# Kernel optimization log

Measured on AMD Instinct MI355X. Metric: run time of the kernel, lower is better.

## Reference

```python
import jax, jax.numpy as jnp
import numpy as np

COMMITMENT_COST = 0.25
NUM_EMBEDDINGS = 512
EMBEDDING_DIM = 64


def setup_inputs() -> dict:
    key = jax.random.key(0)
    k1, k2 = jax.random.split(key)
    inputs = jax.random.normal(k1, (32, EMBEDDING_DIM, 64, 64), dtype=jnp.float32)  # B,C,H,W
    embedding = jax.random.normal(k2, (NUM_EMBEDDINGS, EMBEDDING_DIM), dtype=jnp.float32)  # K,D
    return {"inputs": inputs, "embedding": embedding}


def reference(inputs, embedding):
    # Eval-mode forward of VectorQuantizerEMA (training-branch EMA updates are
    # in-place buffer updates, skipped when self.training is False).
    x = jnp.transpose(inputs, (0, 2, 3, 1))            # B,H,W,C
    B, H, W, D = x.shape
    K = embedding.shape[0]
    flat = x.reshape(-1, D)                            # N,D
    d = (jnp.sum(flat * flat, axis=1, keepdims=True)
         + jnp.sum(embedding * embedding, axis=1)
         - 2.0 * flat @ embedding.T)
    indices = jnp.argmin(d, axis=1)                    # N (int)
    # gather == one-hot @ embedding, but without materializing N x K one-hot
    quantized = embedding[indices].reshape(B, H, W, D)
    # commitment loss (quantized is detached in the torch code)
    e_latent_loss = jnp.mean((jax.lax.stop_gradient(quantized) - x) ** 2)
    loss = COMMITMENT_COST * e_latent_loss
    # straight-through estimator
    quantized_st = x + jax.lax.stop_gradient(quantized - x)
    # perplexity from encoding histogram (avg of one-hots = counts / N)
    counts = jnp.zeros((K,), dtype=flat.dtype).at[indices].add(1.0)
    avg_probs = counts / flat.shape[0]
    perplexity = jnp.exp(-jnp.sum(avg_probs * jnp.log(avg_probs + 1e-10)))
    out = jnp.transpose(quantized_st, (0, 3, 1, 2))    # B,C,H,W
    return loss, out, perplexity, indices
```

## Files before the change

### kernel.cpp

```cpp
#include <hip/hip_runtime.h>
#include <math.h>

#define NPIX   131072
#define KEMB   512
#define DDIM   64
#define HW     4096
#define BSTRIDE 262144

#define OUT_OFF  1
#define PERP_OFF 8388609
#define IDX_OFF  8388610

typedef __attribute__((ext_vector_type(8))) short bf16x8;
typedef __attribute__((ext_vector_type(4))) float f32x4;

__device__ __forceinline__ unsigned short bf16_rtne(float f) {
    unsigned int u = __float_as_uint(f);
    u += 0x7FFFu + ((u >> 16) & 1u);
    return (unsigned short)(u >> 16);
}
__device__ __forceinline__ float bf16_to_f(unsigned short h) {
    return __uint_as_float(((unsigned int)h) << 16);
}

__global__ void vq_init(const float* __restrict__ emb, int* __restrict__ counts,
                        float* __restrict__ hnorms, float* __restrict__ loss_acc,
                        unsigned short* __restrict__ ebh, unsigned short* __restrict__ ebm,
                        unsigned short* __restrict__ ebl) {
    int k = blockIdx.x * 64 + threadIdx.x;
    counts[k] = 0;
    const float4* row4 = (const float4*)(emb + k * DDIM);
    float s = 0.f;
#pragma unroll
    for (int i = 0; i < 16; ++i) {
        float4 v = row4[i];
        s += v.x * v.x + v.y * v.y + v.z * v.z + v.w * v.w;
    }
    hnorms[k] = 0.5f * s;
    const float* row = emb + k * DDIM;
#pragma unroll
    for (int c = 0; c < DDIM; ++c) {
        float x = row[c];
        unsigned short h = bf16_rtne(x);
        float r1 = x - bf16_to_f(h);
        unsigned short m = bf16_rtne(r1);
        float r2 = r1 - bf16_to_f(m);
        unsigned short l = bf16_rtne(r2);
        ebh[k * DDIM + c] = h; ebm[k * DDIM + c] = m; ebl[k * DDIM + c] = l;
    }
    if (k == 0) *loss_acc = 0.f;
}

__global__ __launch_bounds__(256, 2) void vq_main(
    const float* __restrict__ in, const float* __restrict__ emb,
    const unsigned short* __restrict__ ebh, const unsigned short* __restrict__ ebm,
    const unsigned short* __restrict__ ebl,
    const float* __restrict__ hnorms, int* __restrict__ counts,
    float* __restrict__ loss_acc, float* __restrict__ dout)
{
    __shared__ int hist[KEMB];
    const int t = threadIdx.x;
    hist[t] = 0; hist[t + 256] = 0;
    __syncthreads();

    const int lane = t & 63;
    const int wid  = t >> 6;
    const int quad = lane >> 4;
    const int col  = lane & 15;
    const int b    = blockIdx.x >> 4;
    const int p0   = ((blockIdx.x & 15) << 8) | (wid << 6);
    const float* xb = in + b * BSTRIDE;

    bf16x8 xf[3][4][2];
#pragma unroll
    for (int tt = 0; tt < 4; ++tt) {
#pragma unroll
        for (int s = 0; s < 2; ++s) {
            const int pp = p0 + tt * 16 + col;
            const int c0 = s * 32 + quad * 8;
            bf16x8 vh, vm, vl;
#pragma unroll
            for (int j = 0; j < 8; ++j) {
                float x = xb[(c0 + j) * HW + pp];
                unsigned short h = bf16_rtne(x);
                float r1 = x - bf16_to_f(h);
                unsigned short m = bf16_rtne(r1);
                float r2 = r1 - bf16_to_f(m);
                unsigned short l = bf16_rtne(r2);
                vh[j] = (short)h; vm[j] = (short)m; vl[j] = (short)l;
            }
            xf[0][tt][s] = vh; xf[1][tt][s] = vm; xf[2][tt][s] = vl;
        }
    }

    const int arow = col * DDIM + quad * 8;

    float v1[4], v2[4]; int k1[4], k2[4];
#pragma unroll
    for (int tt = 0; tt < 4; ++tt) {
        v1[tt] = 3.402823466e38f; v2[tt] = 3.402823466e38f; k1[tt] = 0; k2[tt] = 0;
    }

#pragma unroll 2
    for (int ct = 0; ct < 32; ++ct) {
        const int off = ct * 16 * DDIM + arow;
        const bf16x8 Ah0 = *(const bf16x8*)(ebh + off);
        const bf16x8 Ah1 = *(const bf16x8*)(ebh + off + 32);
        const bf16x8 Am0 = *(const bf16x8*)(ebm + off);
        const bf16x8 Am1 = *(const bf16x8*)(ebm + off + 32);
        const bf16x8 Al0 = *(const bf16x8*)(ebl + off);
        const bf16x8 Al1 = *(const bf16x8*)(ebl + off + 32);

        f32x4 acc[4];
#pragma unroll
        for (int tt = 0; tt < 4; ++tt) acc[tt] = (f32x4){0.f, 0.f, 0.f, 0.f};

#pragma unroll
        for (int tt = 0; tt < 4; ++tt) {
            acc[tt] = __builtin_amdgcn_mfma_f32_16x16x32_bf16(Ah0, xf[0][tt][0], acc[tt], 0, 0, 0);
            acc[tt] = __builtin_amdgcn_mfma_f32_16x16x32_bf16(Ah0, xf[1][tt][0], acc[tt], 0, 0, 0);
            acc[tt] = __builtin_amdgcn_mfma_f32_16x16x32_bf16(Am0, xf[0][tt][0], acc[tt], 0, 0, 0);
            acc[tt] = __builtin_amdgcn_mfma_f32_16x16x32_bf16(Ah0, xf[2][tt][0], acc[tt], 0, 0, 0);
            acc[tt] = __builtin_amdgcn_mfma_f32_16x16x32_bf16(Al0, xf[0][tt][0], acc[tt], 0, 0, 0);
            acc[tt] = __builtin_amdgcn_mfma_f32_16x16x32_bf16(Am0, xf[1][tt][0], acc[tt], 0, 0, 0);
            acc[tt] = __builtin_amdgcn_mfma_f32_16x16x32_bf16(Ah1, xf[0][tt][1], acc[tt], 0, 0, 0);
            acc[tt] = __builtin_amdgcn_mfma_f32_16x16x32_bf16(Ah1, xf[1][tt][1], acc[tt], 0, 0, 0);
            acc[tt] = __builtin_amdgcn_mfma_f32_16x16x32_bf16(Am1, xf[0][tt][1], acc[tt], 0, 0, 0);
            acc[tt] = __builtin_amdgcn_mfma_f32_16x16x32_bf16(Ah1, xf[2][tt][1], acc[tt], 0, 0, 0);
            acc[tt] = __builtin_amdgcn_mfma_f32_16x16x32_bf16(Al1, xf[0][tt][1], acc[tt], 0, 0, 0);
            acc[tt] = __builtin_amdgcn_mfma_f32_16x16x32_bf16(Am1, xf[1][tt][1], acc[tt], 0, 0, 0);
        }

        const f32x4 hn = *(const f32x4*)(hnorms + ct * 16 + quad * 4);
#pragma unroll
        for (int tt = 0; tt < 4; ++tt) {
#pragma unroll
            for (int r = 0; r < 4; ++r) {
                const float sc = hn[r] - acc[tt][r];
                const int   kk = ct * 16 + quad * 4 + r;
                if (sc < v1[tt]) { v2[tt] = v1[tt]; k2[tt] = k1[tt]; v1[tt] = sc; k1[tt] = kk; }
                else if (sc < v2[tt]) { v2[tt] = sc; k2[tt] = kk; }
            }
        }
    }

#pragma unroll
    for (int tt = 0; tt < 4; ++tt) {
#pragma unroll
        for (int off = 16; off <= 32; off <<= 1) {
            float w1 = __shfl_xor(v1[tt], off, 64); int j1 = __shfl_xor(k1[tt], off, 64);
            float w2 = __shfl_xor(v2[tt], off, 64); int j2 = __shfl_xor(k2[tt], off, 64);
            bool aF = (v1[tt] < w1) || (v1[tt] == w1 && k1[tt] < j1);
            float t1 = aF ? v1[tt] : w1;  int u1 = aF ? k1[tt] : j1;
            float tl = aF ? w1 : v1[tt];  int ul = aF ? j1 : k1[tt];
            bool bS = (v2[tt] < w2) || (v2[tt] == w2 && k2[tt] < j2);
            float tc = bS ? v2[tt] : w2;  int uc = bS ? k2[tt] : j2;
            bool lS = (tl < tc) || (tl == tc && ul < uc);
            v1[tt] = t1; k1[tt] = u1;
            v2[tt] = lS ? tl : tc; k2[tt] = lS ? ul : uc;
        }
    }
    const int kA = k1[quad], kB = k2[quad];
    const int pp = p0 + lane;

    float x[DDIM];
#pragma unroll
    for (int c = 0; c < DDIM; ++c) x[c] = xb[c * HW + pp];

    const float4* eA = (const float4*)(emb + kA * DDIM);
    const float4* eB = (const float4*)(emb + kB * DDIM);
    float a0 = hnorms[kA], a1 = 0.f, a2 = 0.f, a3 = 0.f;
    float b0 = hnorms[kB], b1 = 0.f, b2 = 0.f, b3 = 0.f;
#pragma unroll
    for (int i = 0; i < 16; ++i) {
        float4 ea = eA[i], eb = eB[i];
        const int c = i * 4;
        a0 = fmaf(-x[c + 0], ea.x, a0);
        a1 = fmaf(-x[c + 1], ea.y, a1);
        a2 = fmaf(-x[c + 2], ea.z, a2);
        a3 = fmaf(-x[c + 3], ea.w, a3);
        b0 = fmaf(-x[c + 0], eb.x, b0);
        b1 = fmaf(-x[c + 1], eb.y, b1);
        b2 = fmaf(-x[c + 2], eb.z, b2);
        b3 = fmaf(-x[c + 3], eb.w, b3);
    }
    const float dA = (a0 + a1) + (a2 + a3);
    const float dB = (b0 + b1) + (b2 + b3);
    const int myk = (dB < dA || (dB == dA && kB < kA)) ? kB : kA;

    dout[IDX_OFF + b * HW + pp] = (float)myk;
    atomicAdd(&hist[myk], 1);

    const float4* qrow = (const float4*)(emb + myk * DDIM);
    float* ob = dout + OUT_OFF + b * BSTRIDE;
    float lsum = 0.f;
#pragma unroll
    for (int i = 0; i < 16; ++i) {
        float4 qv = qrow[i];
        const int c = i * 4;
        float d0 = qv.x - x[c + 0];
        float d1 = qv.y - x[c + 1];
        float d2 = qv.z - x[c + 2];
        float d3 = qv.w - x[c + 3];
        lsum += d0 * d0 + d1 * d1 + d2 * d2 + d3 * d3;
        ob[(c + 0) * HW + pp] = x[c + 0] + d0;
        ob[(c + 1) * HW + pp] = x[c + 1] + d1;
        ob[(c + 2) * HW + pp] = x[c + 2] + d2;
        ob[(c + 3) * HW + pp] = x[c + 3] + d3;
    }
    for (int off = 32; off > 0; off >>= 1) lsum += __shfl_down(lsum, off, 64);
    if (lane == 0) atomicAdd(loss_acc, lsum);

    __syncthreads();
    for (int k = t; k < KEMB; k += 256) {
        int v = hist[k];
        if (v) atomicAdd(&counts[k], v);
    }
}

__global__ void vq_fin(const int* __restrict__ counts,
                       const float* __restrict__ loss_acc,
                       float* __restrict__ dout) {
    __shared__ float red[KEMB];
    int k = threadIdx.x;
    float c = (float)counts[k];
    float pa = c / (float)NPIX;
    red[k] = pa * logf(pa + 1e-10f);
    __syncthreads();
    for (int s = 256; s > 0; s >>= 1) {
        if (k < s) red[k] += red[k + s];
        __syncthreads();
    }
    if (k == 0) {
        dout[PERP_OFF] = expf(-red[0]);
        dout[0] = 0.25f * (*loss_acc) / 8388608.0f;
    }
}

extern "C" void kernel_launch(void* const* d_in, const int* in_sizes, int n_in,
                              void* d_out, int out_size, void* d_ws, size_t ws_size,
                              hipStream_t stream) {
    const float* in  = (const float*)d_in[0];
    const float* emb = (const float*)d_in[1];
    float* dout = (float*)d_out;
    int*   counts   = (int*)d_ws;
    float* hnorms   = (float*)((char*)d_ws + 2048);
    float* loss_acc = (float*)((char*)d_ws + 4096);
    unsigned short* ebh = (unsigned short*)((char*)d_ws + 8192);
    unsigned short* ebm = ebh + KEMB * DDIM;
    unsigned short* ebl = ebm + KEMB * DDIM;

    vq_init<<<8, 64, 0, stream>>>(emb, counts, hnorms, loss_acc, ebh, ebm, ebl);
    vq_main<<<512, 256, 0, stream>>>(in, emb, ebh, ebm, ebl, hnorms, counts, loss_acc, dout);
    vq_fin<<<1, 512, 0, stream>>>(counts, loss_acc, dout);
}
```

Baseline: 184.2 us.

## Halve pixels per wave, double grid, prefetch codebook tiles, split refine across lanes

Each wave now handles 32 pixels instead of 64, so the main kernel launches 1024 blocks, and launch bounds are raised to allow 3 blocks per SM. The codebook tile loop is software-pipelined so the next tile's split-bf16 fragments load while the current tile's MFMAs run. The exact fp32 refine of the top two candidates is split across lane halves with a shuffle. vq_init is also parallelized to one thread per element. This trades more blocks and twice the codebook reads per pixel for better occupancy and latency hiding, and half the lanes sit idle during the output write.

```diff
diff --git a/kernel.cpp b/kernel.cpp
--- a/kernel.cpp
+++ b/kernel.cpp
@@ -23,35 +23,38 @@
     return __uint_as_float(((unsigned int)h) << 16);
 }
 
+#define MFMA_STEP(AH, AM, AL, XH, XM, XL, ACC) \
+    ACC = __builtin_amdgcn_mfma_f32_16x16x32_bf16(AH, XH, ACC, 0, 0, 0); \
+    ACC = __builtin_amdgcn_mfma_f32_16x16x32_bf16(AH, XM, ACC, 0, 0, 0); \
+    ACC = __builtin_amdgcn_mfma_f32_16x16x32_bf16(AM, XH, ACC, 0, 0, 0); \
+    ACC = __builtin_amdgcn_mfma_f32_16x16x32_bf16(AH, XL, ACC, 0, 0, 0); \
+    ACC = __builtin_amdgcn_mfma_f32_16x16x32_bf16(AL, XH, ACC, 0, 0, 0); \
+    ACC = __builtin_amdgcn_mfma_f32_16x16x32_bf16(AM, XM, ACC, 0, 0, 0);
+
 __global__ void vq_init(const float* __restrict__ emb, int* __restrict__ counts,
                         float* __restrict__ hnorms, float* __restrict__ loss_acc,
                         unsigned short* __restrict__ ebh, unsigned short* __restrict__ ebm,
                         unsigned short* __restrict__ ebl) {
-    int k = blockIdx.x * 64 + threadIdx.x;
-    counts[k] = 0;
-    const float4* row4 = (const float4*)(emb + k * DDIM);
-    float s = 0.f;
-#pragma unroll
-    for (int i = 0; i < 16; ++i) {
-        float4 v = row4[i];
-        s += v.x * v.x + v.y * v.y + v.z * v.z + v.w * v.w;
-    }
-    hnorms[k] = 0.5f * s;
-    const float* row = emb + k * DDIM;
-#pragma unroll
-    for (int c = 0; c < DDIM; ++c) {
-        float x = row[c];
-        unsigned short h = bf16_rtne(x);
-        float r1 = x - bf16_to_f(h);
-        unsigned short m = bf16_rtne(r1);
-        float r2 = r1 - bf16_to_f(m);
-        unsigned short l = bf16_rtne(r2);
-        ebh[k * DDIM + c] = h; ebm[k * DDIM + c] = m; ebl[k * DDIM + c] = l;
-    }
-    if (k == 0) *loss_acc = 0.f;
-}
-
-__global__ __launch_bounds__(256, 2) void vq_main(
+    const int k = blockIdx.x;
+    const int c = threadIdx.x;
+    float x = emb[k * DDIM + c];
+    unsigned short h = bf16_rtne(x);
+    float r1 = x - bf16_to_f(h);
+    unsigned short m = bf16_rtne(r1);
+    float r2 = r1 - bf16_to_f(m);
+    unsigned short l = bf16_rtne(r2);
+    ebh[k * DDIM + c] = h; ebm[k * DDIM + c] = m; ebl[k * DDIM + c] = l;
+    float s = x * x;
+#pragma unroll
+    for (int off = 1; off <= 32; off <<= 1) s += __shfl_xor(s, off, 64);
+    if (c == 0) {
+        hnorms[k] = 0.5f * s;
+        counts[k] = 0;
+        if (k == 0) *loss_acc = 0.f;
+    }
+}
+
+__global__ __launch_bounds__(256, 3) void vq_main(
     const float* __restrict__ in, const float* __restrict__ emb,
     const unsigned short* __restrict__ ebh, const unsigned short* __restrict__ ebm,
     const unsigned short* __restrict__ ebl,
@@ -67,13 +70,13 @@
     const int wid  = t >> 6;
     const int quad = lane >> 4;
     const int col  = lane & 15;
-    const int b    = blockIdx.x >> 4;
-    const int p0   = ((blockIdx.x & 15) << 8) | (wid << 6);
+    const int b    = blockIdx.x >> 5;
+    const int p0   = ((blockIdx.x & 31) << 7) | (wid << 5);
     const float* xb = in + b * BSTRIDE;
 
-    bf16x8 xf[3][4][2];
-#pragma unroll
-    for (int tt = 0; tt < 4; ++tt) {
+    bf16x8 xf[3][2][2];
+#pragma unroll
+    for (int tt = 0; tt < 2; ++tt) {
 #pragma unroll
         for (int s = 0; s < 2; ++s) {
             const int pp = p0 + tt * 16 + col;
@@ -95,57 +98,76 @@
 
     const int arow = col * DDIM + quad * 8;
 
-    float v1[4], v2[4]; int k1[4], k2[4];
-#pragma unroll
-    for (int tt = 0; tt < 4; ++tt) {
+    float v1[2], v2[2]; int k1[2], k2[2];
+#pragma unroll
+    for (int tt = 0; tt < 2; ++tt) {
         v1[tt] = 3.402823466e38f; v2[tt] = 3.402823466e38f; k1[tt] = 0; k2[tt] = 0;
     }
 
-#pragma unroll 2
-    for (int ct = 0; ct < 32; ++ct) {
-        const int off = ct * 16 * DDIM + arow;
-        const bf16x8 Ah0 = *(const bf16x8*)(ebh + off);
-        const bf16x8 Ah1 = *(const bf16x8*)(ebh + off + 32);
-        const bf16x8 Am0 = *(const bf16x8*)(ebm + off);
-        const bf16x8 Am1 = *(const bf16x8*)(ebm + off + 32);
-        const bf16x8 Al0 = *(const bf16x8*)(ebl + off);
-        const bf16x8 Al1 = *(const bf16x8*)(ebl + off + 32);
-
-        f32x4 acc[4];
-#pragma unroll
-        for (int tt = 0; tt < 4; ++tt) acc[tt] = (f32x4){0.f, 0.f, 0.f, 0.f};
-
-#pragma unroll
-        for (int tt = 0; tt < 4; ++tt) {
-            acc[tt] = __builtin_amdgcn_mfma_f32_16x16x32_bf16(Ah0, xf[0][tt][0], acc[tt], 0, 0, 0);
-            acc[tt] = __builtin_amdgcn_mfma_f32_16x16x32_bf16(Ah0, xf[1][tt][0], acc[tt], 0, 0, 0);
-            acc[tt] = __builtin_amdgcn_mfma_f32_16x16x32_bf16(Am0, xf[0][tt][0], acc[tt], 0, 0, 0);
-            acc[tt] = __builtin_amdgcn_mfma_f32_16x16x32_bf16(Ah0, xf[2][tt][0], acc[tt], 0, 0, 0);
-            acc[tt] = __builtin_amdgcn_mfma_f32_16x16x32_bf16(Al0, xf[0][tt][0], acc[tt], 0, 0, 0);
-            acc[tt] = __builtin_amdgcn_mfma_f32_16x16x32_bf16(Am0, xf[1][tt][0], acc[tt], 0, 0, 0);
-            acc[tt] = __builtin_amdgcn_mfma_f32_16x16x32_bf16(Ah1, xf[0][tt][1], acc[tt], 0, 0, 0);
-            acc[tt] = __builtin_amdgcn_mfma_f32_16x16x32_bf16(Ah1, xf[1][tt][1], acc[tt], 0, 0, 0);
-            acc[tt] = __builtin_amdgcn_mfma_f32_16x16x32_bf16(Am1, xf[0][tt][1], acc[tt], 0, 0, 0);
-            acc[tt] = __builtin_amdgcn_mfma_f32_16x16x32_bf16(Ah1, xf[2][tt][1], acc[tt], 0, 0, 0);
-            acc[tt] = __builtin_amdgcn_mfma_f32_16x16x32_bf16(Al1, xf[0][tt][1], acc[tt], 0, 0, 0);
-            acc[tt] = __builtin_amdgcn_mfma_f32_16x16x32_bf16(Am1, xf[1][tt][1], acc[tt], 0, 0, 0);
-        }
-
-        const f32x4 hn = *(const f32x4*)(hnorms + ct * 16 + quad * 4);
-#pragma unroll
-        for (int tt = 0; tt < 4; ++tt) {
-#pragma unroll
-            for (int r = 0; r < 4; ++r) {
-                const float sc = hn[r] - acc[tt][r];
-                const int   kk = ct * 16 + quad * 4 + r;
-                if (sc < v1[tt]) { v2[tt] = v1[tt]; k2[tt] = k1[tt]; v1[tt] = sc; k1[tt] = kk; }
-                else if (sc < v2[tt]) { v2[tt] = sc; k2[tt] = kk; }
-            }
-        }
-    }
-
-#pragma unroll
-    for (int tt = 0; tt < 4; ++tt) {
+    bf16x8 Ah0 = *(const bf16x8*)(ebh + arow);
+    bf16x8 Ah1 = *(const bf16x8*)(ebh + arow + 32);
+    bf16x8 Am0 = *(const bf16x8*)(ebm + arow);
+    bf16x8 Am1 = *(const bf16x8*)(ebm + arow + 32);
+    bf16x8 Al0 = *(const bf16x8*)(ebl + arow);
+    bf16x8 Al1 = *(const bf16x8*)(ebl + arow + 32);
+    f32x4 hnA = *(const f32x4*)(hnorms + quad * 4);
+
+    for (int ct = 0; ct < 32; ct += 2) {
+        const int offB = (ct + 1) * (16 * DDIM) + arow;
+        const bf16x8 Bh0 = *(const bf16x8*)(ebh + offB);
+        const bf16x8 Bh1 = *(const bf16x8*)(ebh + offB + 32);
+        const bf16x8 Bm0 = *(const bf16x8*)(ebm + offB);
+        const bf16x8 Bm1 = *(const bf16x8*)(ebm + offB + 32);
+        const bf16x8 Bl0 = *(const bf16x8*)(ebl + offB);
+        const bf16x8 Bl1 = *(const bf16x8*)(ebl + offB + 32);
+        const f32x4 hnB = *(const f32x4*)(hnorms + (ct + 1) * 16 + quad * 4);
+
+        f32x4 acc0 = (f32x4){0.f, 0.f, 0.f, 0.f};
+        f32x4 acc1 = (f32x4){0.f, 0.f, 0.f, 0.f};
+        MFMA_STEP(Ah0, Am0, Al0, xf[0][0][0], xf[1][0][0], xf[2][0][0], acc0)
+        MFMA_STEP(Ah1, Am1, Al1, xf[0][0][1], xf[1][0][1], xf[2][0][1], acc0)
+        MFMA_STEP(Ah0, Am0, Al0, xf[0][1][0], xf[1][1][0], xf[2][1][0], acc1)
+        MFMA_STEP(Ah1, Am1, Al1, xf[0][1][1], xf[1][1][1], xf[2][1][1], acc1)
+#pragma unroll
+        for (int r = 0; r < 4; ++r) {
+            const int kk = ct * 16 + quad * 4 + r;
+            float sc = hnA[r] - acc0[r];
+            if (sc < v1[0]) { v2[0] = v1[0]; k2[0] = k1[0]; v1[0] = sc; k1[0] = kk; }
+            else if (sc < v2[0]) { v2[0] = sc; k2[0] = kk; }
+            sc = hnA[r] - acc1[r];
+            if (sc < v1[1]) { v2[1] = v1[1]; k2[1] = k1[1]; v1[1] = sc; k1[1] = kk; }
+            else if (sc < v2[1]) { v2[1] = sc; k2[1] = kk; }
+        }
+
+        const int offA = (((ct + 2) & 31)) * (16 * DDIM) + arow;
+        Ah0 = *(const bf16x8*)(ebh + offA);
+        Ah1 = *(const bf16x8*)(ebh + offA + 32);
+        Am0 = *(const bf16x8*)(ebm + offA);
+        Am1 = *(const bf16x8*)(ebm + offA + 32);
+        Al0 = *(const bf16x8*)(ebl + offA);
+        Al1 = *(const bf16x8*)(ebl + offA + 32);
+        hnA = *(const f32x4*)(hnorms + ((ct + 2) & 31) * 16 + quad * 4);
+
+        acc0 = (f32x4){0.f, 0.f, 0.f, 0.f};
+        acc1 = (f32x4){0.f, 0.f, 0.f, 0.f};
+        MFMA_STEP(Bh0, Bm0, Bl0, xf[0][0][0], xf[1][0][0], xf[2][0][0], acc0)
+        MFMA_STEP(Bh1, Bm1, Bl1, xf[0][0][1], xf[1][0][1], xf[2][0][1], acc0)
+        MFMA_STEP(Bh0, Bm0, Bl0, xf[0][1][0], xf[1][1][0], xf[2][1][0], acc1)
+        MFMA_STEP(Bh1, Bm1, Bl1, xf[0][1][1], xf[1][1][1], xf[2][1][1], acc1)
+#pragma unroll
+        for (int r = 0; r < 4; ++r) {
+            const int kk = (ct + 1) * 16 + quad * 4 + r;
+            float sc = hnB[r] - acc0[r];
+            if (sc < v1[0]) { v2[0] = v1[0]; k2[0] = k1[0]; v1[0] = sc; k1[0] = kk; }
+            else if (sc < v2[0]) { v2[0] = sc; k2[0] = kk; }
+            sc = hnB[r] - acc1[r];
+            if (sc < v1[1]) { v2[1] = v1[1]; k2[1] = k1[1]; v1[1] = sc; k1[1] = kk; }
+            else if (sc < v2[1]) { v2[1] = sc; k2[1] = kk; }
+        }
+    }
+
+#pragma unroll
+    for (int tt = 0; tt < 2; ++tt) {
 #pragma unroll
         for (int off = 16; off <= 32; off <<= 1) {
             float w1 = __shfl_xor(v1[tt], off, 64); int j1 = __shfl_xor(k1[tt], off, 64);
@@ -160,53 +182,55 @@
             v2[tt] = lS ? tl : tc; k2[tt] = lS ? ul : uc;
         }
     }
-    const int kA = k1[quad], kB = k2[quad];
-    const int pp = p0 + lane;
+
+    const int q    = lane & 31;
+    const int pp   = p0 + q;
+    const int tsel = (lane >> 4) & 1;
+    const int kA = tsel ? k1[1] : k1[0];
+    const int kB = tsel ? k2[1] : k2[0];
 
     float x[DDIM];
 #pragma unroll
     for (int c = 0; c < DDIM; ++c) x[c] = xb[c * HW + pp];
 
-    const float4* eA = (const float4*)(emb + kA * DDIM);
-    const float4* eB = (const float4*)(emb + kB * DDIM);
-    float a0 = hnorms[kA], a1 = 0.f, a2 = 0.f, a3 = 0.f;
-    float b0 = hnorms[kB], b1 = 0.f, b2 = 0.f, b3 = 0.f;
+    const int kMine = (lane < 32) ? kA : kB;
+    const float4* eM = (const float4*)(emb + kMine * DDIM);
+    float a0 = hnorms[kMine], a1 = 0.f, a2 = 0.f, a3 = 0.f;
 #pragma unroll
     for (int i = 0; i < 16; ++i) {
-        float4 ea = eA[i], eb = eB[i];
+        float4 ea = eM[i];
         const int c = i * 4;
         a0 = fmaf(-x[c + 0], ea.x, a0);
         a1 = fmaf(-x[c + 1], ea.y, a1);
         a2 = fmaf(-x[c + 2], ea.z, a2);
         a3 = fmaf(-x[c + 3], ea.w, a3);
-        b0 = fmaf(-x[c + 0], eb.x, b0);
-        b1 = fmaf(-x[c + 1], eb.y, b1);
-        b2 = fmaf(-x[c + 2], eb.z, b2);
-        b3 = fmaf(-x[c + 3], eb.w, b3);
-    }
-    const float dA = (a0 + a1) + (a2 + a3);
-    const float dB = (b0 + b1) + (b2 + b3);
+    }
+    const float dMine = (a0 + a1) + (a2 + a3);
+    const float dOth  = __shfl_xor(dMine, 32, 64);
+    const float dA = (lane < 32) ? dMine : dOth;
+    const float dB = (lane < 32) ? dOth  : dMine;
     const int myk = (dB < dA || (dB == dA && kB < kA)) ? kB : kA;
 
-    dout[IDX_OFF + b * HW + pp] = (float)myk;
-    atomicAdd(&hist[myk], 1);
-
-    const float4* qrow = (const float4*)(emb + myk * DDIM);
-    float* ob = dout + OUT_OFF + b * BSTRIDE;
     float lsum = 0.f;
-#pragma unroll
-    for (int i = 0; i < 16; ++i) {
-        float4 qv = qrow[i];
-        const int c = i * 4;
-        float d0 = qv.x - x[c + 0];
-        float d1 = qv.y - x[c + 1];
-        float d2 = qv.z - x[c + 2];
-        float d3 = qv.w - x[c + 3];
-        lsum += d0 * d0 + d1 * d1 + d2 * d2 + d3 * d3;
-        ob[(c + 0) * HW + pp] = x[c + 0] + d0;
-        ob[(c + 1) * HW + pp] = x[c + 1] + d1;
-        ob[(c + 2) * HW + pp] = x[c + 2] + d2;
-        ob[(c + 3) * HW + pp] = x[c + 3] + d3;
+    if (lane < 32) {
+        dout[IDX_OFF + b * HW + pp] = (float)myk;
+        atomicAdd(&hist[myk], 1);
+        const float4* qrow = (const float4*)(emb + myk * DDIM);
+        float* ob = dout + OUT_OFF + b * BSTRIDE;
+#pragma unroll
+        for (int i = 0; i < 16; ++i) {
+            float4 qv = qrow[i];
+            const int c = i * 4;
+            float d0 = qv.x - x[c + 0];
+            float d1 = qv.y - x[c + 1];
+            float d2 = qv.z - x[c + 2];
+            float d3 = qv.w - x[c + 3];
+            lsum += d0 * d0 + d1 * d1 + d2 * d2 + d3 * d3;
+            ob[(c + 0) * HW + pp] = x[c + 0] + d0;
+            ob[(c + 1) * HW + pp] = x[c + 1] + d1;
+            ob[(c + 2) * HW + pp] = x[c + 2] + d2;
+            ob[(c + 3) * HW + pp] = x[c + 3] + d3;
+        }
     }
     for (int off = 32; off > 0; off >>= 1) lsum += __shfl_down(lsum, off, 64);
     if (lane == 0) atomicAdd(loss_acc, lsum);
@@ -250,7 +274,7 @@
     unsigned short* ebm = ebh + KEMB * DDIM;
     unsigned short* ebl = ebm + KEMB * DDIM;
 
-    vq_init<<<8, 64, 0, stream>>>(emb, counts, hnorms, loss_acc, ebh, ebm, ebl);
-    vq_main<<<512, 256, 0, stream>>>(in, emb, ebh, ebm, ebl, hnorms, counts, loss_acc, dout);
+    vq_init<<<512, 64, 0, stream>>>(emb, counts, hnorms, loss_acc, ebh, ebm, ebl);
+    vq_main<<<1024, 256, 0, stream>>>(in, emb, ebh, ebm, ebl, hnorms, counts, loss_acc, dout);
     vq_fin<<<1, 512, 0, stream>>>(counts, loss_acc, dout);
 }
```

Result: slower. 237.3 us (+28.9%).

## Stage codebook tiles in double-buffered LDS and parallelize codebook prep kernel

Applied to the files above, without the earlier changes.

The main kernel now cooperatively loads each 16-entry codebook tile (hi/mid/lo bf16 splits) into a double-buffered shared-memory tile, prefetching the next tile into registers while MFMAs run on the current one. Half-norms are also cached in LDS. This replaces per-wave redundant global/L2 loads of the codebook with one shared load per block. The prep kernel is rewritten to use one block per embedding row with a wave-shuffle norm reduction, which gives it far more parallelism. The cost is an added __syncthreads per tile iteration and more LDS per block, which could reduce occupancy.

```diff
diff --git a/kernel.cpp b/kernel.cpp
--- a/kernel.cpp
+++ b/kernel.cpp
@@ -23,32 +23,35 @@
     return __uint_as_float(((unsigned int)h) << 16);
 }
 
+#define MFMA_STEP(AH, AM, AL, XH, XM, XL, ACC) \
+    ACC = __builtin_amdgcn_mfma_f32_16x16x32_bf16(AH, XH, ACC, 0, 0, 0); \
+    ACC = __builtin_amdgcn_mfma_f32_16x16x32_bf16(AH, XM, ACC, 0, 0, 0); \
+    ACC = __builtin_amdgcn_mfma_f32_16x16x32_bf16(AM, XH, ACC, 0, 0, 0); \
+    ACC = __builtin_amdgcn_mfma_f32_16x16x32_bf16(AH, XL, ACC, 0, 0, 0); \
+    ACC = __builtin_amdgcn_mfma_f32_16x16x32_bf16(AL, XH, ACC, 0, 0, 0); \
+    ACC = __builtin_amdgcn_mfma_f32_16x16x32_bf16(AM, XM, ACC, 0, 0, 0);
+
 __global__ void vq_init(const float* __restrict__ emb, int* __restrict__ counts,
                         float* __restrict__ hnorms, float* __restrict__ loss_acc,
                         unsigned short* __restrict__ ebh, unsigned short* __restrict__ ebm,
                         unsigned short* __restrict__ ebl) {
-    int k = blockIdx.x * 64 + threadIdx.x;
-    counts[k] = 0;
-    const float4* row4 = (const float4*)(emb + k * DDIM);
-    float s = 0.f;
-#pragma unroll
-    for (int i = 0; i < 16; ++i) {
-        float4 v = row4[i];
-        s += v.x * v.x + v.y * v.y + v.z * v.z + v.w * v.w;
-    }
-    hnorms[k] = 0.5f * s;
-    const float* row = emb + k * DDIM;
-#pragma unroll
-    for (int c = 0; c < DDIM; ++c) {
-        float x = row[c];
-        unsigned short h = bf16_rtne(x);
-        float r1 = x - bf16_to_f(h);
-        unsigned short m = bf16_rtne(r1);
-        float r2 = r1 - bf16_to_f(m);
-        unsigned short l = bf16_rtne(r2);
-        ebh[k * DDIM + c] = h; ebm[k * DDIM + c] = m; ebl[k * DDIM + c] = l;
-    }
-    if (k == 0) *loss_acc = 0.f;
+    const int k = blockIdx.x;
+    const int c = threadIdx.x;
+    float x = emb[k * DDIM + c];
+    unsigned short h = bf16_rtne(x);
+    float r1 = x - bf16_to_f(h);
+    unsigned short m = bf16_rtne(r1);
+    float r2 = r1 - bf16_to_f(m);
+    unsigned short l = bf16_rtne(r2);
+    ebh[k * DDIM + c] = h; ebm[k * DDIM + c] = m; ebl[k * DDIM + c] = l;
+    float s = x * x;
+#pragma unroll
+    for (int off = 1; off <= 32; off <<= 1) s += __shfl_xor(s, off, 64);
+    if (c == 0) {
+        hnorms[k] = 0.5f * s;
+        counts[k] = 0;
+        if (k == 0) *loss_acc = 0.f;
+    }
 }
 
 __global__ __launch_bounds__(256, 2) void vq_main(
@@ -59,9 +62,12 @@
     float* __restrict__ loss_acc, float* __restrict__ dout)
 {
     __shared__ int hist[KEMB];
+    __shared__ __align__(16) float hn_lds[KEMB];
+    __shared__ __align__(16) unsigned short atile[2][3072];
+
     const int t = threadIdx.x;
     hist[t] = 0; hist[t + 256] = 0;
-    __syncthreads();
+    if (t < 128) ((float4*)hn_lds)[t] = ((const float4*)hnorms)[t];
 
     const int lane = t & 63;
     const int wid  = t >> 6;
@@ -70,6 +76,14 @@
     const int b    = blockIdx.x >> 4;
     const int p0   = ((blockIdx.x & 15) << 8) | (wid << 6);
     const float* xb = in + b * BSTRIDE;
+
+    const int s1  = t >> 7;
+    const int ks  = (t >> 6) & 1;
+    const int lf  = t & 63;
+    const unsigned short* tab1 = s1 ? ebm : ebh;
+    const int src_off = (lf & 15) * 64 + ks * 32 + (lf >> 4) * 8;
+    const int dst1 = s1 * 1024 + ks * 512 + lf * 8;
+    const int dst2 = 2 * 1024 + ks * 512 + lf * 8;
 
     bf16x8 xf[3][4][2];
 #pragma unroll
@@ -93,7 +107,9 @@
         }
     }
 
-    const int arow = col * DDIM + quad * 8;
+    *(bf16x8*)&atile[0][dst1] = *(const bf16x8*)(tab1 + src_off);
+    if (t < 128) *(bf16x8*)&atile[0][dst2] = *(const bf16x8*)(ebl + src_off);
+    __syncthreads();
 
     float v1[4], v2[4]; int k1[4], k2[4];
 #pragma unroll
@@ -101,37 +117,33 @@
         v1[tt] = 3.402823466e38f; v2[tt] = 3.402823466e38f; k1[tt] = 0; k2[tt] = 0;
     }
 
-#pragma unroll 2
     for (int ct = 0; ct < 32; ++ct) {
-        const int off = ct * 16 * DDIM + arow;
-        const bf16x8 Ah0 = *(const bf16x8*)(ebh + off);
-        const bf16x8 Ah1 = *(const bf16x8*)(ebh + off + 32);
-        const bf16x8 Am0 = *(const bf16x8*)(ebm + off);
-        const bf16x8 Am1 = *(const bf16x8*)(ebm + off + 32);
-        const bf16x8 Al0 = *(const bf16x8*)(ebl + off);
-        const bf16x8 Al1 = *(const bf16x8*)(ebl + off + 32);
+        const int cur = ct & 1;
+        bf16x8 g1, g2;
+        if (ct < 31) {
+            const int sb = (ct + 1) * 1024 + src_off;
+            g1 = *(const bf16x8*)(tab1 + sb);
+            if (t < 128) g2 = *(const bf16x8*)(ebl + sb);
+        }
+
+        const unsigned short* abuf = atile[cur];
+        const bf16x8 Ah0 = *(const bf16x8*)&abuf[           lane * 8];
+        const bf16x8 Ah1 = *(const bf16x8*)&abuf[ 512 +     lane * 8];
+        const bf16x8 Am0 = *(const bf16x8*)&abuf[1024 +     lane * 8];
+        const bf16x8 Am1 = *(const bf16x8*)&abuf[1536 +     lane * 8];
+        const bf16x8 Al0 = *(const bf16x8*)&abuf[2048 +     lane * 8];
+        const bf16x8 Al1 = *(const bf16x8*)&abuf[2560 +     lane * 8];
 
         f32x4 acc[4];
 #pragma unroll
         for (int tt = 0; tt < 4; ++tt) acc[tt] = (f32x4){0.f, 0.f, 0.f, 0.f};
-
 #pragma unroll
         for (int tt = 0; tt < 4; ++tt) {
-            acc[tt] = __builtin_amdgcn_mfma_f32_16x16x32_bf16(Ah0, xf[0][tt][0], acc[tt], 0, 0, 0);
-            acc[tt] = __builtin_amdgcn_mfma_f32_16x16x32_bf16(Ah0, xf[1][tt][0], acc[tt], 0, 0, 0);
-            acc[tt] = __builtin_amdgcn_mfma_f32_16x16x32_bf16(Am0, xf[0][tt][0], acc[tt], 0, 0, 0);
-            acc[tt] = __builtin_amdgcn_mfma_f32_16x16x32_bf16(Ah0, xf[2][tt][0], acc[tt], 0, 0, 0);
-            acc[tt] = __builtin_amdgcn_mfma_f32_16x16x32_bf16(Al0, xf[0][tt][0], acc[tt], 0, 0, 0);
-            acc[tt] = __builtin_amdgcn_mfma_f32_16x16x32_bf16(Am0, xf[1][tt][0], acc[tt], 0, 0, 0);
-            acc[tt] = __builtin_amdgcn_mfma_f32_16x16x32_bf16(Ah1, xf[0][tt][1], acc[tt], 0, 0, 0);
-            acc[tt] = __builtin_amdgcn_mfma_f32_16x16x32_bf16(Ah1, xf[1][tt][1], acc[tt], 0, 0, 0);
-            acc[tt] = __builtin_amdgcn_mfma_f32_16x16x32_bf16(Am1, xf[0][tt][1], acc[tt], 0, 0, 0);
-            acc[tt] = __builtin_amdgcn_mfma_f32_16x16x32_bf16(Ah1, xf[2][tt][1], acc[tt], 0, 0, 0);
-            acc[tt] = __builtin_amdgcn_mfma_f32_16x16x32_bf16(Al1, xf[0][tt][1], acc[tt], 0, 0, 0);
-            acc[tt] = __builtin_amdgcn_mfma_f32_16x16x32_bf16(Am1, xf[1][tt][1], acc[tt], 0, 0, 0);
-        }
-
-        const f32x4 hn = *(const f32x4*)(hnorms + ct * 16 + quad * 4);
+            MFMA_STEP(Ah0, Am0, Al0, xf[0][tt][0], xf[1][tt][0], xf[2][tt][0], acc[tt])
+            MFMA_STEP(Ah1, Am1, Al1, xf[0][tt][1], xf[1][tt][1], xf[2][tt][1], acc[tt])
+        }
+
+        const f32x4 hn = *(const f32x4*)&hn_lds[ct * 16 + quad * 4];
 #pragma unroll
         for (int tt = 0; tt < 4; ++tt) {
 #pragma unroll
@@ -142,6 +154,13 @@
                 else if (sc < v2[tt]) { v2[tt] = sc; k2[tt] = kk; }
             }
         }
+
+        if (ct < 31) {
+            const int nxt = cur ^ 1;
+            *(bf16x8*)&atile[nxt][dst1] = g1;
+            if (t < 128) *(bf16x8*)&atile[nxt][dst2] = g2;
+        }
+        __syncthreads();
     }
 
 #pragma unroll
@@ -169,8 +188,8 @@
 
     const float4* eA = (const float4*)(emb + kA * DDIM);
     const float4* eB = (const float4*)(emb + kB * DDIM);
-    float a0 = hnorms[kA], a1 = 0.f, a2 = 0.f, a3 = 0.f;
-    float b0 = hnorms[kB], b1 = 0.f, b2 = 0.f, b3 = 0.f;
+    float a0 = hn_lds[kA], a1 = 0.f, a2 = 0.f, a3 = 0.f;
+    float b0 = hn_lds[kB], b1 = 0.f, b2 = 0.f, b3 = 0.f;
 #pragma unroll
     for (int i = 0; i < 16; ++i) {
         float4 ea = eA[i], eb = eB[i];
@@ -250,7 +269,7 @@
     unsigned short* ebm = ebh + KEMB * DDIM;
     unsigned short* ebl = ebm + KEMB * DDIM;
 
-    vq_init<<<8, 64, 0, stream>>>(emb, counts, hnorms, loss_acc, ebh, ebm, ebl);
+    vq_init<<<512, 64, 0, stream>>>(emb, counts, hnorms, loss_acc, ebh, ebm, ebl);
     vq_main<<<512, 256, 0, stream>>>(in, emb, ebh, ebm, ebl, hnorms, counts, loss_acc, dout);
     vq_fin<<<1, 512, 0, stream>>>(counts, loss_acc, dout);
 }
```

Result: faster. 180.2 us (-2.1%).
